# Performance work log

Measured on AMD Instinct MI355X. Metric: run time of the kernel, lower is better.

The kernel has to match this reference:

```python
import jax, jax.numpy as jnp
import numpy as np

N = 8192
D_IN = 256
D_OUT = 256
DROP_P = 0.5


def setup_inputs() -> dict:
    key = jax.random.key(0)
    k1, k2, k3, k4, k5 = jax.random.split(key, 5)
    inputs = jax.random.normal(k1, (N, D_IN), dtype=jnp.float32)
    # torch nn.Linear weights are [d_out, d_in], applied as x @ W.T
    Wq = jax.random.normal(k2, (D_OUT, D_IN), dtype=jnp.float32) * (1.0 / np.sqrt(D_IN))
    Wk = jax.random.normal(k3, (D_OUT, D_IN), dtype=jnp.float32) * (1.0 / np.sqrt(D_IN))
    Wv = jax.random.normal(k4, (D_OUT, D_IN), dtype=jnp.float32) * (1.0 / np.sqrt(D_IN))
    # deterministic dropout keep-mask (True = keep), p=0.5
    drop_mask = jax.random.bernoulli(k5, 1.0 - DROP_P, (N, N))
    return {"inputs": inputs, "Wq": Wq, "Wk": Wk, "Wv": Wv, "drop_mask": drop_mask}


def reference(inputs, Wq, Wk, Wv, drop_mask):
    # QKV projections (no bias)
    q = inputs @ Wq.T  # [N, d_out]
    k = inputs @ Wk.T  # [N, d_out]
    v = inputs @ Wv.T  # [N, d_out]

    d_k = k.shape[1]
    scores = q @ k.T  # [N, N]

    # causal mask: strictly-upper-triangular entries -> -inf
    n = scores.shape[0]
    causal = jnp.triu(jnp.ones((n, n), dtype=bool), k=1)
    masked = jnp.where(causal, -jnp.inf, scores)

    attn_weights = jax.nn.softmax(masked / jnp.sqrt(jnp.float32(d_k)), axis=-1)

    # dropout p=0.5 in train mode: zero dropped entries, scale kept by 1/(1-p)
    scale = jnp.float32(1.0 / (1.0 - DROP_P))
    attn_weights = jnp.where(drop_mask, attn_weights * scale, 0.0)

    context_vector = attn_weights @ v  # [N, d_out]
    return context_vector
```

## Files before the change

### kernel.cpp

```cpp
#include <hip/hip_runtime.h>

#define NT 8192
#define DM 256

typedef float f32x16 __attribute__((ext_vector_type(16)));
typedef float f32x4 __attribute__((ext_vector_type(4)));
typedef __bf16 bf16x8 __attribute__((ext_vector_type(8)));

#define MFMA32(a, b, c) __builtin_amdgcn_mfma_f32_32x32x16_bf16((a), (b), (c), 0, 0, 0)
#define MFMA16(a, b, c) __builtin_amdgcn_mfma_f32_16x16x32_bf16((a), (b), (c), 0, 0, 0)
#define NEG_INF (-__builtin_inff())

static __device__ __forceinline__ unsigned short f2bf_bits(float f) {
  return __builtin_bit_cast(unsigned short, (__bf16)f);
}
static __device__ __forceinline__ float exp2_fast(float x) {
  return __builtin_amdgcn_exp2f(x);
}
static __device__ __forceinline__ void gload_lds16(const void* g, void* l) {
  __builtin_amdgcn_global_load_lds(
      (const __attribute__((address_space(1))) unsigned int*)g,
      (__attribute__((address_space(3))) unsigned int*)l, 16, 0, 0);
}

__global__ void detect_kernel(const unsigned int* __restrict__ m, int* __restrict__ flag) {
  __shared__ int s01, sf;
  int t = threadIdx.x;
  if (t == 0) { s01 = 1; sf = 1; }
  __syncthreads();
  unsigned int v = m[t];
  if (v > 1u) atomicAnd(&s01, 0);
  if (v != 0u && v != 0x3F800000u) atomicAnd(&sf, 0);
  __syncthreads();
  if (t == 0) *flag = s01 ? 1 : (sf ? 2 : 0);
}

__global__ __launch_bounds__(256) void maskpack_kernel(
    const void* __restrict__ mask, const int* __restrict__ flagp,
    unsigned long long* __restrict__ bm) {
  const int t = threadIdx.x, lane = t & 63, w = t >> 6;
  const int r = blockIdx.x + (w << 11);
  const int mode = *flagp;
  const int jmax = ((r >> 6) + 1) << 6;
  unsigned long long* out = bm + (size_t)r * 128;
  if (mode == 0) {
    const unsigned char* mk = (const unsigned char*)mask + (size_t)r * NT;
    for (int j = 0; j < jmax; j += 64) {
      unsigned long long b = __ballot(mk[j + lane] != 0);
      if (lane == 0) out[j >> 6] = b;
    }
  } else {
    const unsigned int* mk = (const unsigned int*)mask + (size_t)r * NT;
    for (int j = 0; j < jmax; j += 64) {
      unsigned long long b = __ballot(mk[j + lane] != 0u);
      if (lane == 0) out[j >> 6] = b;
    }
  }
}

__global__ __launch_bounds__(256) void proj_kernel(
    const float* __restrict__ X, const float* __restrict__ Wq,
    const float* __restrict__ Wk, const float* __restrict__ Wv,
    unsigned short* __restrict__ Qs, unsigned short* __restrict__ Kb,
    unsigned short* __restrict__ Vt) {
  __shared__ __align__(16) unsigned short Xs[64 * 256];
  __shared__ __align__(16) unsigned short Ws[64 * 256];
  __shared__ float Tr[4][32 * 33];
  const int ib = blockIdx.x, mat = blockIdx.y;
  const float* W = (mat == 0) ? Wq : (mat == 1) ? Wk : Wv;
  const float wscale = (mat == 0) ? 0.09016844005556021f : 1.0f;
  const int t = threadIdx.x;
  const int lane = t & 63, w = t >> 6;
  const int m = lane & 31, half = lane >> 5;
  const int i0 = ib * 64;
#pragma unroll
  for (int cc = 0; cc < 8; ++cc) {
    int chunk = t + 256 * cc;
    int rr = chunk >> 5, c = chunk & 31;
    const float4* src = (const float4*)(X + (size_t)(i0 + rr) * 256 + c * 8);
    float4 f0 = src[0], f1 = src[1];
    bf16x8 v;
    v[0] = (__bf16)f0.x; v[1] = (__bf16)f0.y; v[2] = (__bf16)f0.z; v[3] = (__bf16)f0.w;
    v[4] = (__bf16)f1.x; v[5] = (__bf16)f1.y; v[6] = (__bf16)f1.z; v[7] = (__bf16)f1.w;
    *(bf16x8*)&Xs[(rr * 32 + (c ^ (rr & 31))) * 8] = v;
  }
  const int wr = w >> 1, wc = w & 1;
  for (int cb = 0; cb < 4; ++cb) {
    __syncthreads();
#pragma unroll
    for (int cc = 0; cc < 8; ++cc) {
      int chunk = t + 256 * cc;
      int rr = chunk >> 5, c = chunk & 31;
      const float4* src = (const float4*)(W + (size_t)(cb * 64 + rr) * 256 + c * 8);
      float4 f0 = src[0], f1 = src[1];
      bf16x8 v;
      v[0] = (__bf16)(f0.x * wscale); v[1] = (__bf16)(f0.y * wscale);
      v[2] = (__bf16)(f0.z * wscale); v[3] = (__bf16)(f0.w * wscale);
      v[4] = (__bf16)(f1.x * wscale); v[5] = (__bf16)(f1.y * wscale);
      v[6] = (__bf16)(f1.z * wscale); v[7] = (__bf16)(f1.w * wscale);
      *(bf16x8*)&Ws[(rr * 32 + (c ^ (rr & 31))) * 8] = v;
    }
    __syncthreads();
    f32x16 acc = {};
    const int ar = 32 * wr + m;
    const int br = 32 * wc + m;
#pragma unroll
    for (int st = 0; st < 16; ++st) {
      int kc = st * 2 + half;
      bf16x8 a = *(const bf16x8*)&Xs[(ar * 32 + (kc ^ (ar & 31))) * 8];
      bf16x8 b = *(const bf16x8*)&Ws[(br * 32 + (kc ^ (br & 31))) * 8];
      acc = MFMA32(a, b, acc);
    }
    if (mat < 2) {
      unsigned short* O = mat ? Kb : Qs;
#pragma unroll
      for (int r = 0; r < 16; ++r) {
        int row = i0 + 32 * wr + (r & 3) + 8 * (r >> 2) + 4 * half;
        int col = cb * 64 + 32 * wc + m;
        O[(size_t)row * DM + col] = f2bf_bits(acc[r]);
      }
    } else {
      float* T = Tr[w];
#pragma unroll
      for (int r = 0; r < 16; ++r) {
        int rl = (r & 3) + 8 * (r >> 2) + 4 * half;
        T[m * 33 + rl] = acc[r];
      }
      asm volatile("s_waitcnt lgkmcnt(0)" ::: "memory");
#pragma unroll
      for (int q = 0; q < 16; ++q) {
        int dl = 2 * q + half;
        float val = T[dl * 33 + m];
        Vt[(size_t)(cb * 64 + 32 * wc + dl) * NT + i0 + 32 * wr + m] = f2bf_bits(val);
      }
      asm volatile("s_waitcnt lgkmcnt(0)" ::: "memory");
    }
  }
}

__global__ __launch_bounds__(256, 3) void flash_kernel(
    const unsigned short* __restrict__ Qs, const unsigned short* __restrict__ Kg,
    const unsigned short* __restrict__ Vtg, const unsigned int* __restrict__ bm,
    float* __restrict__ ml_out, unsigned short* __restrict__ acc_out) {
  __shared__ __align__(16) unsigned short Ksh[32 * 256];
  __shared__ __align__(16) unsigned short Vsh[256 * 32];
  __shared__ __align__(16) unsigned short Psh[4][16 * 32];
  const int ib = blockIdx.x;
  const int seg = blockIdx.y;
  const int jb_end = 2 * (ib + 1);
  const int jb0 = seg * 16;
  if (jb0 >= jb_end) return;
  const int jb1 = (jb0 + 16 < jb_end) ? jb0 + 16 : jb_end;
  const int t = threadIdx.x, lane = t & 63, w = t >> 6;
  const int m = lane & 15, q = lane >> 4;
  const int i0 = ib * 64, rw0 = i0 + 16 * w;
  const int myrow = rw0 + m;

  bf16x8 qf[8];
  {
    const unsigned short* qp = Qs + (size_t)myrow * DM + q * 8;
#pragma unroll
    for (int st = 0; st < 8; ++st) qf[st] = *(const bf16x8*)(qp + st * 32);
  }
  f32x4 oacc[16] = {};
  float mrun = -1e30f, lrun = 0.f;

  for (int jb = jb0; jb < jb1; ++jb) {
    const int j32 = jb * 32;
#pragma unroll
    for (int i = 0; i < 4; ++i) {
      int chunk = t + 256 * i;
      int row = chunk >> 5, slot = chunk & 31;
      int gc = slot ^ row;
      gload_lds16(Kg + (size_t)(j32 + row) * DM + gc * 8, Ksh + (size_t)chunk * 8);
    }
#pragma unroll
    for (int i = 0; i < 4; ++i) {
      int chunk = t + 256 * i;
      int d = chunk >> 2, slot = chunk & 3;
      int gj = slot ^ (d & 3);
      gload_lds16(Vtg + (size_t)d * NT + j32 + gj * 8, Vsh + (size_t)chunk * 8);
    }
    __syncthreads();
    if (j32 <= rw0 + 15) {
      unsigned int bits = bm[(size_t)myrow * 256 + (j32 >> 5)];
      f32x4 s[2] = {};
#pragma unroll
      for (int st = 0; st < 8; ++st) {
        int kc = st * 4 + q;
#pragma unroll
        for (int ct = 0; ct < 2; ++ct) {
          int jr = ct * 16 + m;
          bf16x8 a = *(const bf16x8*)&Ksh[(jr * 32 + (kc ^ jr)) * 8];
          s[ct] = MFMA16(a, qf[st], s[ct]);
        }
      }
      if (j32 + 31 > rw0) {
#pragma unroll
        for (int ct = 0; ct < 2; ++ct)
#pragma unroll
          for (int r = 0; r < 4; ++r)
            if (j32 + ct * 16 + q * 4 + r > myrow) s[ct][r] = NEG_INF;
      }
      float mx = fmaxf(fmaxf(fmaxf(s[0][0], s[0][1]), fmaxf(s[0][2], s[0][3])),
                       fmaxf(fmaxf(s[1][0], s[1][1]), fmaxf(s[1][2], s[1][3])));
      mx = fmaxf(mx, __shfl_xor(mx, 16));
      mx = fmaxf(mx, __shfl_xor(mx, 32));
      float mn = fmaxf(mrun, mx);
      float alpha = exp2_fast(mrun - mn);
      mrun = mn;
#pragma unroll
      for (int ct = 0; ct < 2; ++ct)
#pragma unroll
        for (int r = 0; r < 4; ++r) s[ct][r] = exp2_fast(s[ct][r] - mn);
      float rs = (s[0][0] + s[0][1]) + (s[0][2] + s[0][3]) +
                 (s[1][0] + s[1][1]) + (s[1][2] + s[1][3]);
      rs += __shfl_xor(rs, 16);
      rs += __shfl_xor(rs, 32);
      lrun = lrun * alpha + rs;
#pragma unroll
      for (int ct = 0; ct < 16; ++ct)
#pragma unroll
        for (int r = 0; r < 4; ++r) oacc[ct][r] *= alpha;
      unsigned short* P = Psh[w];
#pragma unroll
      for (int ct = 0; ct < 2; ++ct) {
        unsigned int bb = bits >> (ct * 16 + q * 4);
        unsigned long long pk = 0;
#pragma unroll
        for (int r = 0; r < 4; ++r) {
          float pv = ((bb >> r) & 1u) ? s[ct][r] * 2.0f : 0.0f;
          pk |= (unsigned long long)f2bf_bits(pv) << (16 * r);
        }
        int c = ct * 2 + (q >> 1);
        *(unsigned long long*)&P[m * 32 + ((c ^ (m & 3)) << 3) + ((q & 1) << 2)] = pk;
      }
      asm volatile("s_waitcnt lgkmcnt(0)" ::: "memory");
      bf16x8 pf = *(const bf16x8*)&P[m * 32 + ((q ^ (m & 3)) << 3)];
#pragma unroll
      for (int ct = 0; ct < 16; ++ct) {
        int d = ct * 16 + m;
        bf16x8 a = *(const bf16x8*)&Vsh[(d * 4 + (q ^ (d & 3))) * 8];
        oacc[ct] = MFMA16(a, pf, oacc[ct]);
      }
    }
    __syncthreads();
  }
  const int a_ = ib >> 3, r_ = ib & 7;
  const int g = 4 * a_ * (a_ + 1) + r_ * (a_ + 1) + seg;
  if (q == 0) {
    float* mlb = ml_out + ((size_t)g * 64 + 16 * w + m) * 2;
    mlb[0] = mrun;
    mlb[1] = lrun;
  }
  unsigned short* ab = acc_out + ((size_t)g * 64 + 16 * w + m) * DM;
#pragma unroll
  for (int ct = 0; ct < 16; ++ct) {
    unsigned long long pk = 0;
#pragma unroll
    for (int r = 0; r < 4; ++r)
      pk |= (unsigned long long)f2bf_bits(oacc[ct][r]) << (16 * r);
    *(unsigned long long*)&ab[ct * 16 + q * 4] = pk;
  }
}

__global__ __launch_bounds__(256) void combine_kernel(
    const float* __restrict__ ml, const unsigned short* __restrict__ pacc,
    float* __restrict__ out) {
  const int t = threadIdx.x;
  const int row = blockIdx.x * 32 + (t >> 3);
  const int cg = (t & 7) * 32;
  const int ib = row >> 6, rib = row & 63;
  const int a = ib >> 3, r = ib & 7;
  const int g0 = 4 * a * (a + 1) + r * (a + 1);
  const int ns = a + 1;
  float M = -1e30f;
  for (int s = 0; s < ns; ++s) M = fmaxf(M, ml[((size_t)(g0 + s) * 64 + rib) * 2]);
  float Wd = 0.f;
  float acc[32];
#pragma unroll
  for (int j = 0; j < 32; ++j) acc[j] = 0.f;
  for (int s = 0; s < ns; ++s) {
    const float* mls = ml + ((size_t)(g0 + s) * 64 + rib) * 2;
    float wv = exp2_fast(mls[0] - M);
    Wd += wv * mls[1];
    const unsigned short* pa = pacc + ((size_t)(g0 + s) * 64 + rib) * DM + cg;
#pragma unroll
    for (int v4 = 0; v4 < 4; ++v4) {
      bf16x8 b = *(const bf16x8*)(pa + v4 * 8);
#pragma unroll
      for (int j = 0; j < 8; ++j) acc[v4 * 8 + j] += wv * (float)b[j];
    }
  }
  float inv = 1.0f / Wd;
#pragma unroll
  for (int j = 0; j < 32; ++j) out[(size_t)row * DM + cg + j] = acc[j] * inv;
}

extern "C" void kernel_launch(void* const* d_in, const int* in_sizes, int n_in,
                              void* d_out, int out_size, void* d_ws, size_t ws_size,
                              hipStream_t stream) {
  const float* X  = (const float*)d_in[0];
  const float* Wq = (const float*)d_in[1];
  const float* Wk = (const float*)d_in[2];
  const float* Wv = (const float*)d_in[3];
  const void* mask = d_in[4];
  float* out = (float*)d_out;

  char* ws = (char*)d_ws;
  int* flag = (int*)ws;
  unsigned short* Qs = (unsigned short*)(ws + 4096);
  unsigned short* Kb = Qs + (size_t)NT * DM;
  unsigned short* Vt = Kb + (size_t)NT * DM;
  float* ml = (float*)(Vt + (size_t)NT * DM);
  unsigned short* pacc = (unsigned short*)(ml + (size_t)1088 * 64 * 2);
  unsigned long long* bmw = (unsigned long long*)((char*)pacc + (size_t)1088 * 64 * DM * 2);

  detect_kernel<<<1, 256, 0, stream>>>((const unsigned int*)mask, flag);
  maskpack_kernel<<<2048, 256, 0, stream>>>(mask, flag, bmw);
  proj_kernel<<<dim3(128, 3), 256, 0, stream>>>(X, Wq, Wk, Wv, Qs, Kb, Vt);
  flash_kernel<<<dim3(128, 16), 256, 0, stream>>>(Qs, Kb, Vt, (const unsigned int*)bmw,
                                                  ml, pacc);
  combine_kernel<<<256, 256, 0, stream>>>(ml, pacc, out);
}
```

Baseline: 527.4 us.

## Rework flash kernel with 32x32 MFMA tiles, 128-row blocks, and double-buffered K/V

The flash attention kernel now handles 128 query rows per block, 32 per wave, using 32x32x16 MFMA instead of 16x16x32. K/V tiles are double-buffered in LDS so the next tile's loads overlap compute. The P matrix moves between MFMA layouts through register shuffles instead of an LDS round trip. The dropout scale of 2 is folded into the V projection weights. Rescaling of the output accumulator is skipped when the running max is unchanged. Occupancy drops to 2 blocks per CU and the partial-result indexing in combine is updated to match.

Measured after the change: 565.6 us. +7.2%, slower.

```diff
diff --git a/kernel.cpp b/kernel.cpp
--- a/kernel.cpp
+++ b/kernel.cpp
@@ -4,11 +4,10 @@
 #define DM 256
 
 typedef float f32x16 __attribute__((ext_vector_type(16)));
-typedef float f32x4 __attribute__((ext_vector_type(4)));
 typedef __bf16 bf16x8 __attribute__((ext_vector_type(8)));
+typedef unsigned int u32x4 __attribute__((ext_vector_type(4)));
 
 #define MFMA32(a, b, c) __builtin_amdgcn_mfma_f32_32x32x16_bf16((a), (b), (c), 0, 0, 0)
-#define MFMA16(a, b, c) __builtin_amdgcn_mfma_f32_16x16x32_bf16((a), (b), (c), 0, 0, 0)
 #define NEG_INF (-__builtin_inff())
 
 static __device__ __forceinline__ unsigned short f2bf_bits(float f) {
@@ -68,7 +67,7 @@
   __shared__ float Tr[4][32 * 33];
   const int ib = blockIdx.x, mat = blockIdx.y;
   const float* W = (mat == 0) ? Wq : (mat == 1) ? Wk : Wv;
-  const float wscale = (mat == 0) ? 0.09016844005556021f : 1.0f;
+  const float wscale = (mat == 0) ? 0.09016844005556021f : (mat == 2 ? 2.0f : 1.0f);
   const int t = threadIdx.x;
   const int lane = t & 63, w = t >> 6;
   const int m = lane & 31, half = lane >> 5;
@@ -138,130 +137,155 @@
   }
 }
 
-__global__ __launch_bounds__(256, 3) void flash_kernel(
+__global__ __launch_bounds__(256, 2) void flash_kernel(
     const unsigned short* __restrict__ Qs, const unsigned short* __restrict__ Kg,
     const unsigned short* __restrict__ Vtg, const unsigned int* __restrict__ bm,
     float* __restrict__ ml_out, unsigned short* __restrict__ acc_out) {
-  __shared__ __align__(16) unsigned short Ksh[32 * 256];
-  __shared__ __align__(16) unsigned short Vsh[256 * 32];
-  __shared__ __align__(16) unsigned short Psh[4][16 * 32];
-  const int ib = blockIdx.x;
-  const int seg = blockIdx.y;
-  const int jb_end = 2 * (ib + 1);
+  __shared__ __align__(16) unsigned short Ksh[2][32 * 256];
+  __shared__ __align__(16) unsigned short Vsh[2][256 * 32];
+  const int ib = blockIdx.x, seg = blockIdx.y;
+  const int jb_end = 4 * (ib + 1);
   const int jb0 = seg * 16;
   if (jb0 >= jb_end) return;
   const int jb1 = (jb0 + 16 < jb_end) ? jb0 + 16 : jb_end;
   const int t = threadIdx.x, lane = t & 63, w = t >> 6;
-  const int m = lane & 15, q = lane >> 4;
-  const int i0 = ib * 64, rw0 = i0 + 16 * w;
-  const int myrow = rw0 + m;
-
-  bf16x8 qf[8];
+  const int il = lane & 31, h = lane >> 5;
+  const int i0 = ib * 128, rw0 = i0 + 32 * w;
+  const int myrow = rw0 + il;
+
+  bf16x8 qf[16];
   {
-    const unsigned short* qp = Qs + (size_t)myrow * DM + q * 8;
-#pragma unroll
-    for (int st = 0; st < 8; ++st) qf[st] = *(const bf16x8*)(qp + st * 32);
-  }
-  f32x4 oacc[16] = {};
+    const unsigned short* qp = Qs + (size_t)myrow * DM + 8 * h;
+#pragma unroll
+    for (int st = 0; st < 16; ++st) qf[st] = *(const bf16x8*)(qp + st * 16);
+  }
+  f32x16 oacc[8] = {};
   float mrun = -1e30f, lrun = 0.f;
 
+#define STAGE(JB, B)                                                          \
+  {                                                                           \
+    const int j32_ = (JB) * 32;                                               \
+    _Pragma("unroll") for (int i_ = 0; i_ < 4; ++i_) {                        \
+      int chunk = t + 256 * i_;                                               \
+      int row = chunk >> 5, slot = chunk & 31;                                \
+      gload_lds16(Kg + (size_t)(j32_ + row) * DM + (slot ^ row) * 8,          \
+                  &Ksh[B][(size_t)chunk * 8]);                                \
+    }                                                                         \
+    _Pragma("unroll") for (int i_ = 0; i_ < 4; ++i_) {                        \
+      int chunk = t + 256 * i_;                                               \
+      int d_ = chunk >> 2, slot = chunk & 3;                                  \
+      gload_lds16(Vtg + (size_t)d_ * NT + j32_ + (slot ^ ((d_ >> 1) & 3)) * 8,\
+                  &Vsh[B][(size_t)chunk * 8]);                                \
+    }                                                                         \
+  }
+
+  STAGE(jb0, 0)
   for (int jb = jb0; jb < jb1; ++jb) {
+    const int buf = (jb - jb0) & 1;
     const int j32 = jb * 32;
-#pragma unroll
-    for (int i = 0; i < 4; ++i) {
-      int chunk = t + 256 * i;
-      int row = chunk >> 5, slot = chunk & 31;
-      int gc = slot ^ row;
-      gload_lds16(Kg + (size_t)(j32 + row) * DM + gc * 8, Ksh + (size_t)chunk * 8);
-    }
-#pragma unroll
-    for (int i = 0; i < 4; ++i) {
-      int chunk = t + 256 * i;
-      int d = chunk >> 2, slot = chunk & 3;
-      int gj = slot ^ (d & 3);
-      gload_lds16(Vtg + (size_t)d * NT + j32 + gj * 8, Vsh + (size_t)chunk * 8);
-    }
-    __syncthreads();
-    if (j32 <= rw0 + 15) {
-      unsigned int bits = bm[(size_t)myrow * 256 + (j32 >> 5)];
-      f32x4 s[2] = {};
-#pragma unroll
-      for (int st = 0; st < 8; ++st) {
-        int kc = st * 4 + q;
-#pragma unroll
-        for (int ct = 0; ct < 2; ++ct) {
-          int jr = ct * 16 + m;
-          bf16x8 a = *(const bf16x8*)&Ksh[(jr * 32 + (kc ^ jr)) * 8];
-          s[ct] = MFMA16(a, qf[st], s[ct]);
+    __builtin_amdgcn_s_barrier();
+    unsigned int bits = bm[(size_t)myrow * 256 + (j32 >> 5)];
+    if (jb + 1 < jb1) {
+      STAGE(jb + 1, buf ^ 1)
+      asm volatile("s_waitcnt vmcnt(8)" ::: "memory");
+    } else {
+      asm volatile("s_waitcnt vmcnt(0)" ::: "memory");
+    }
+    __builtin_amdgcn_s_barrier();
+    if (j32 <= rw0 + 31) {
+      const unsigned short* Kb_ = Ksh[buf];
+      const unsigned short* Vb_ = Vsh[buf];
+      f32x16 s = {};
+#pragma unroll
+      for (int st = 0; st < 16; ++st) {
+        int c = (2 * st + h) ^ il;
+        bf16x8 a = *(const bf16x8*)&Kb_[(il * 32 + c) * 8];
+        s = MFMA32(a, qf[st], s);
+      }
+      if (j32 + 31 > myrow) {
+#pragma unroll
+        for (int r = 0; r < 16; ++r) {
+          int J = (r & 3) + 8 * (r >> 2) + 4 * h;
+          if (j32 + J > myrow) s[r] = NEG_INF;
         }
       }
-      if (j32 + 31 > rw0) {
-#pragma unroll
-        for (int ct = 0; ct < 2; ++ct)
-#pragma unroll
-          for (int r = 0; r < 4; ++r)
-            if (j32 + ct * 16 + q * 4 + r > myrow) s[ct][r] = NEG_INF;
-      }
-      float mx = fmaxf(fmaxf(fmaxf(s[0][0], s[0][1]), fmaxf(s[0][2], s[0][3])),
-                       fmaxf(fmaxf(s[1][0], s[1][1]), fmaxf(s[1][2], s[1][3])));
-      mx = fmaxf(mx, __shfl_xor(mx, 16));
+      float mx = s[0];
+#pragma unroll
+      for (int r = 1; r < 16; ++r) mx = fmaxf(mx, s[r]);
       mx = fmaxf(mx, __shfl_xor(mx, 32));
-      float mn = fmaxf(mrun, mx);
-      float alpha = exp2_fast(mrun - mn);
-      mrun = mn;
-#pragma unroll
-      for (int ct = 0; ct < 2; ++ct)
-#pragma unroll
-        for (int r = 0; r < 4; ++r) s[ct][r] = exp2_fast(s[ct][r] - mn);
-      float rs = (s[0][0] + s[0][1]) + (s[0][2] + s[0][3]) +
-                 (s[1][0] + s[1][1]) + (s[1][2] + s[1][3]);
-      rs += __shfl_xor(rs, 16);
+      const float mn = fmaxf(mrun, mx);
+#pragma unroll
+      for (int r = 0; r < 16; ++r) s[r] = exp2_fast(s[r] - mn);
+      float rs = 0.f;
+#pragma unroll
+      for (int r = 0; r < 16; ++r) rs += s[r];
       rs += __shfl_xor(rs, 32);
-      lrun = lrun * alpha + rs;
-#pragma unroll
-      for (int ct = 0; ct < 16; ++ct)
-#pragma unroll
-        for (int r = 0; r < 4; ++r) oacc[ct][r] *= alpha;
-      unsigned short* P = Psh[w];
-#pragma unroll
-      for (int ct = 0; ct < 2; ++ct) {
-        unsigned int bb = bits >> (ct * 16 + q * 4);
-        unsigned long long pk = 0;
-#pragma unroll
-        for (int r = 0; r < 4; ++r) {
-          float pv = ((bb >> r) & 1u) ? s[ct][r] * 2.0f : 0.0f;
-          pk |= (unsigned long long)f2bf_bits(pv) << (16 * r);
-        }
-        int c = ct * 2 + (q >> 1);
-        *(unsigned long long*)&P[m * 32 + ((c ^ (m & 3)) << 3) + ((q & 1) << 2)] = pk;
-      }
-      asm volatile("s_waitcnt lgkmcnt(0)" ::: "memory");
-      bf16x8 pf = *(const bf16x8*)&P[m * 32 + ((q ^ (m & 3)) << 3)];
-#pragma unroll
-      for (int ct = 0; ct < 16; ++ct) {
-        int d = ct * 16 + m;
-        bf16x8 a = *(const bf16x8*)&Vsh[(d * 4 + (q ^ (d & 3))) * 8];
-        oacc[ct] = MFMA16(a, pf, oacc[ct]);
-      }
-    }
-    __syncthreads();
-  }
-  const int a_ = ib >> 3, r_ = ib & 7;
-  const int g = 4 * a_ * (a_ + 1) + r_ * (a_ + 1) + seg;
-  if (q == 0) {
-    float* mlb = ml_out + ((size_t)g * 64 + 16 * w + m) * 2;
+      if (__all(mn == mrun)) {
+        lrun += rs;
+      } else {
+        float alpha = exp2_fast(mrun - mn);
+        lrun = lrun * alpha + rs;
+#pragma unroll
+        for (int ct = 0; ct < 8; ++ct)
+#pragma unroll
+          for (int r = 0; r < 16; ++r) oacc[ct][r] *= alpha;
+        mrun = mn;
+      }
+      unsigned int dw[8];
+#pragma unroll
+      for (int tt = 0; tt < 4; ++tt) {
+        unsigned int bb = bits >> (8 * tt + 4 * h);
+        float v0 = (bb & 1u) ? s[4 * tt + 0] : 0.f;
+        float v1 = (bb & 2u) ? s[4 * tt + 1] : 0.f;
+        float v2 = (bb & 4u) ? s[4 * tt + 2] : 0.f;
+        float v3 = (bb & 8u) ? s[4 * tt + 3] : 0.f;
+        dw[2 * tt] = (unsigned)f2bf_bits(v0) | ((unsigned)f2bf_bits(v1) << 16);
+        dw[2 * tt + 1] = (unsigned)f2bf_bits(v2) | ((unsigned)f2bf_bits(v3) << 16);
+      }
+      unsigned int x0 = __shfl_xor(h ? dw[0] : dw[2], 32);
+      unsigned int x1 = __shfl_xor(h ? dw[1] : dw[3], 32);
+      unsigned int x2 = __shfl_xor(h ? dw[4] : dw[6], 32);
+      unsigned int x3 = __shfl_xor(h ? dw[5] : dw[7], 32);
+      u32x4 pw0, pw1;
+      if (h == 0) {
+        pw0 = (u32x4){dw[0], dw[1], x0, x1};
+        pw1 = (u32x4){dw[4], dw[5], x2, x3};
+      } else {
+        pw0 = (u32x4){x0, x1, dw[2], dw[3]};
+        pw1 = (u32x4){x2, x3, dw[6], dw[7]};
+      }
+      bf16x8 pf0 = __builtin_bit_cast(bf16x8, pw0);
+      bf16x8 pf1 = __builtin_bit_cast(bf16x8, pw1);
+#pragma unroll
+      for (int ct = 0; ct < 8; ++ct) {
+        int d0 = ct * 32 + il;
+        int sw = (d0 >> 1) & 3;
+        bf16x8 a0 = *(const bf16x8*)&Vb_[(d0 * 4 + (h ^ sw)) * 8];
+        oacc[ct] = MFMA32(a0, pf0, oacc[ct]);
+        bf16x8 a1 = *(const bf16x8*)&Vb_[(d0 * 4 + ((h + 2) ^ sw)) * 8];
+        oacc[ct] = MFMA32(a1, pf1, oacc[ct]);
+      }
+    }
+  }
+#undef STAGE
+  const int a_ = ib >> 2, r_ = ib & 3;
+  const int g = 2 * a_ * (a_ + 1) + r_ * (a_ + 1) + seg;
+  if (h == 0) {
+    float* mlb = ml_out + ((size_t)g * 128 + 32 * w + il) * 2;
     mlb[0] = mrun;
     mlb[1] = lrun;
   }
-  unsigned short* ab = acc_out + ((size_t)g * 64 + 16 * w + m) * DM;
-#pragma unroll
-  for (int ct = 0; ct < 16; ++ct) {
-    unsigned long long pk = 0;
-#pragma unroll
-    for (int r = 0; r < 4; ++r)
-      pk |= (unsigned long long)f2bf_bits(oacc[ct][r]) << (16 * r);
-    *(unsigned long long*)&ab[ct * 16 + q * 4] = pk;
-  }
+  unsigned short* ab = acc_out + ((size_t)g * 128 + 32 * w + il) * DM;
+#pragma unroll
+  for (int ct = 0; ct < 8; ++ct)
+#pragma unroll
+    for (int tt = 0; tt < 4; ++tt) {
+      unsigned int lo = (unsigned)f2bf_bits(oacc[ct][4 * tt + 0]) |
+                        ((unsigned)f2bf_bits(oacc[ct][4 * tt + 1]) << 16);
+      unsigned int hi = (unsigned)f2bf_bits(oacc[ct][4 * tt + 2]) |
+                        ((unsigned)f2bf_bits(oacc[ct][4 * tt + 3]) << 16);
+      *(uint2*)&ab[ct * 32 + 8 * tt + 4 * h] = make_uint2(lo, hi);
+    }
 }
 
 __global__ __launch_bounds__(256) void combine_kernel(
@@ -270,21 +294,21 @@
   const int t = threadIdx.x;
   const int row = blockIdx.x * 32 + (t >> 3);
   const int cg = (t & 7) * 32;
-  const int ib = row >> 6, rib = row & 63;
-  const int a = ib >> 3, r = ib & 7;
-  const int g0 = 4 * a * (a + 1) + r * (a + 1);
+  const int ib = row >> 7, rib = row & 127;
+  const int a = ib >> 2, r = ib & 3;
+  const int g0 = 2 * a * (a + 1) + r * (a + 1);
   const int ns = a + 1;
   float M = -1e30f;
-  for (int s = 0; s < ns; ++s) M = fmaxf(M, ml[((size_t)(g0 + s) * 64 + rib) * 2]);
+  for (int s = 0; s < ns; ++s) M = fmaxf(M, ml[((size_t)(g0 + s) * 128 + rib) * 2]);
   float Wd = 0.f;
   float acc[32];
 #pragma unroll
   for (int j = 0; j < 32; ++j) acc[j] = 0.f;
   for (int s = 0; s < ns; ++s) {
-    const float* mls = ml + ((size_t)(g0 + s) * 64 + rib) * 2;
+    const float* mls = ml + ((size_t)(g0 + s) * 128 + rib) * 2;
     float wv = exp2_fast(mls[0] - M);
     Wd += wv * mls[1];
-    const unsigned short* pa = pacc + ((size_t)(g0 + s) * 64 + rib) * DM + cg;
+    const unsigned short* pa = pacc + ((size_t)(g0 + s) * 128 + rib) * DM + cg;
 #pragma unroll
     for (int v4 = 0; v4 < 4; ++v4) {
       bf16x8 b = *(const bf16x8*)(pa + v4 * 8);
@@ -313,13 +337,13 @@
   unsigned short* Kb = Qs + (size_t)NT * DM;
   unsigned short* Vt = Kb + (size_t)NT * DM;
   float* ml = (float*)(Vt + (size_t)NT * DM);
-  unsigned short* pacc = (unsigned short*)(ml + (size_t)1088 * 64 * 2);
-  unsigned long long* bmw = (unsigned long long*)((char*)pacc + (size_t)1088 * 64 * DM * 2);
+  unsigned short* pacc = (unsigned short*)(ml + (size_t)544 * 128 * 2);
+  unsigned long long* bmw = (unsigned long long*)((char*)pacc + (size_t)544 * 128 * DM * 2);
 
   detect_kernel<<<1, 256, 0, stream>>>((const unsigned int*)mask, flag);
   maskpack_kernel<<<2048, 256, 0, stream>>>(mask, flag, bmw);
   proj_kernel<<<dim3(128, 3), 256, 0, stream>>>(X, Wq, Wk, Wv, Qs, Kb, Vt);
-  flash_kernel<<<dim3(128, 16), 256, 0, stream>>>(Qs, Kb, Vt, (const unsigned int*)bmw,
-                                                  ml, pacc);
+  flash_kernel<<<dim3(64, 16), 256, 0, stream>>>(Qs, Kb, Vt, (const unsigned int*)bmw,
+                                                 ml, pacc);
   combine_kernel<<<256, 256, 0, stream>>>(ml, pacc, out);
 }
```
